# Kernel optimization log

Hardware: AMD Instinct MI355X
Metric: run time of the kernel (lower is better)

## Reference

```python
import math
import jax, jax.numpy as jnp
import numpy as np

N_HEADS = 16
D_HEAD = 128
D_ROPE = 64  # d_head // 2
ROPE_SCALE = 40.0


def _rotate_half(x):
    x1, x2 = jnp.split(x, 2, axis=-1)
    return jnp.concatenate([-x2, x1], axis=-1)


def _apply_rotary(x, cos, sin):
    # rotate only the first cos.shape[-1] dims of the rope slice
    half = cos.shape[-1]
    x_rot, x_base = x[..., :half], x[..., half:]
    x_rot = x_rot * cos + _rotate_half(x_rot) * sin
    return jnp.concatenate([x_rot, x_base], axis=-1)


def _forward(x, W_dkv, W_dq, W_uk, W_uv, W_uq, W_kr, W_qr, W_out):
    B, S, H = x.shape
    c_kv = x @ W_dkv                                   # [B,S,cd]
    c_q = x @ W_dq                                     # [B,S,cd]
    q_c = c_q @ W_uq                                   # [B,S,up]
    k_c = c_kv @ W_uk                                  # [B,S,up]
    v = (c_kv @ W_uv).reshape(B, S, N_HEADS, D_HEAD)   # [B,S,h,d]
    k_r = (x @ W_kr).reshape(B, S, N_HEADS, D_ROPE)
    q_r = (q_c @ W_qr).reshape(B, S, N_HEADS, D_ROPE)

    # RoPE (partial: first d_rope//2 dims rotated, rest passthrough)
    half_dim = D_ROPE // 2
    inv_freq = 1.0 / (10000.0 ** (jnp.arange(0, half_dim, 2, dtype=jnp.float32) / half_dim))
    t = jnp.arange(S, dtype=jnp.float32) / ROPE_SCALE
    freqs = jnp.einsum('i,j->ij', t, inv_freq)         # [S, d_rope//4]
    rotation = jnp.concatenate([freqs, freqs], axis=-1)  # [S, d_rope//2]
    cos = jnp.cos(rotation)[None, :, None, :]
    sin = jnp.sin(rotation)[None, :, None, :]
    k_rope = _apply_rotary(k_r, cos, sin)
    q_rope = _apply_rotary(q_r, cos, sin)

    k = jnp.concatenate([k_c.reshape(B, S, N_HEADS, D_HEAD - D_ROPE), k_rope], axis=-1)
    q = jnp.concatenate([q_c.reshape(B, S, N_HEADS, D_HEAD - D_ROPE), q_rope], axis=-1)

    # NOTE: faithful to source: einsum takes (k, q) in that order, and the
    # softmax result is computed but UNUSED (AV uses raw scores). Replicated.
    scores = jnp.einsum('bihd,bjhd->bhij', k, q) / math.sqrt(D_HEAD)
    out = jnp.einsum('bhij,bjhd->bihd', scores, v)     # [B,S,h,d]
    output = out.reshape(B, S, N_HEADS * D_HEAD) @ W_out
    return output, c_kv, k_rope


def setup_inputs() -> dict:
    key = jax.random.key(0)
    ks = jax.random.split(key, 9)
    B, S, H, CD, UP = 2, 2048, 2048, 1024, 1024
    w = lambda k, shp: jax.random.normal(k, shp, dtype=jnp.float32) * 0.02
    return {
        'x': jax.random.normal(ks[0], (B, S, H), dtype=jnp.float32),
        'W_dkv': w(ks[1], (H, CD)),
        'W_dq': w(ks[2], (H, CD)),
        'W_uk': w(ks[3], (CD, UP)),
        'W_uv': w(ks[4], (CD, N_HEADS * D_HEAD)),
        'W_uq': w(ks[5], (CD, UP)),
        'W_kr': w(ks[6], (H, N_HEADS * D_ROPE)),
        'W_qr': w(ks[7], (CD, N_HEADS * D_ROPE)),
        'W_out': w(ks[8], (N_HEADS * D_HEAD, H)),
    }


def reference(x, W_dkv, W_dq, W_uk, W_uv, W_uq, W_kr, W_qr, W_out):
    return _forward(x, W_dkv, W_dq, W_uk, W_uv, W_uq, W_kr, W_qr, W_out)
```

## Files before the change

kernel.cpp:

```cpp
#include <hip/hip_runtime.h>
#include <math.h>

typedef _Float16 half8 __attribute__((ext_vector_type(8)));
typedef float floatx4 __attribute__((ext_vector_type(4)));

typedef const uint32_t __attribute__((address_space(1)))* gp1_t;
typedef uint32_t __attribute__((address_space(3)))* lp3_t;
#define GLDS16(g, l) __builtin_amdgcn_global_load_lds((gp1_t)(const void*)(g), (lp3_t)(void*)(l), 16, 0, 0)

#define BK 32

#define BARRIER() __builtin_amdgcn_s_barrier()
#define VM8()     asm volatile("s_waitcnt vmcnt(8)" ::: "memory")

__device__ inline int xcd_swz(int wg, int nwg)
{
    int q = nwg >> 3, r = nwg & 7;
    int xcd = wg & 7, idx = wg >> 3;
    return (xcd < r) ? (xcd * (q + 1) + idx) : (r * (q + 1) + (xcd - r) * q + idx);
}

__global__ __launch_bounds__(256) void gemm_fast(
    const _Float16* __restrict__ A, const _Float16* __restrict__ B,
    float* __restrict__ Cf, _Float16* __restrict__ Ch,
    float* __restrict__ Cx, _Float16* __restrict__ Cy,
    int Kc, long lda, long ldb, long ldcf, long ldch,
    int cmap, long cf_lo, long cf_hi, float alpha, int nh, int nsk, int epi_mode,
    long aoff_b, long aoff_h, long boff_b, long boff_h,
    long coff_b, long coff_h, long coff_s)
{
    __shared__ __align__(16) _Float16 As[128 * BK];
    __shared__ __align__(16) _Float16 Bs[128 * BK];

    const int z = blockIdx.z;
    const int hs = nh * nsk;
    const int zb = z / hs;
    const int rr = z % hs;
    const int zh = rr / nsk;
    const int ks = rr % nsk;

    const _Float16* Ab = A + (long)zb * aoff_b + (long)zh * aoff_h + (long)ks * Kc;
    const _Float16* Bb = B + (long)zb * boff_b + (long)zh * boff_h + (long)ks * Kc;
    const long cofs = (long)zb * coff_b + (long)zh * coff_h + (long)ks * coff_s;

    const int nwg = gridDim.x * gridDim.y;
    const int swz = xcd_swz(blockIdx.y * gridDim.x + blockIdx.x, nwg);
    const long m0 = (long)(swz / gridDim.x) * 128;
    const long n0 = (long)(swz % gridDim.x) * 128;
    const int t = threadIdx.x;
    const int wave = t >> 6, lane = t & 63;
    const int lr = lane & 15, lq = lane >> 4;
    const int wm = (wave & 1) * 64, wn = (wave >> 1) * 64;

    const int c0 = wave * 64 + lane;
    const int c1 = c0 + 256;
    const _Float16* ga0 = Ab + (m0 + (c0 >> 2)) * lda + (c0 & 3) * 8;
    const _Float16* ga1 = Ab + (m0 + (c1 >> 2)) * lda + (c1 & 3) * 8;
    const _Float16* gb0 = Bb + (n0 + (c0 >> 2)) * ldb + (c0 & 3) * 8;
    const _Float16* gb1 = Bb + (n0 + (c1 >> 2)) * ldb + (c1 & 3) * 8;
    _Float16* lA0 = As + wave * 512;
    _Float16* lA1 = As + 2048 + wave * 512;
    _Float16* lB0 = Bs + wave * 512;
    _Float16* lB1 = Bs + 2048 + wave * 512;

    floatx4 acc[4][4];
    #pragma unroll
    for (int i = 0; i < 4; ++i)
        #pragma unroll
        for (int j = 0; j < 4; ++j) acc[i][j] = (floatx4){0.f, 0.f, 0.f, 0.f};

    for (int k0 = 0; k0 < Kc; k0 += BK) {
        GLDS16(ga0, lA0); GLDS16(ga1, lA1);
        GLDS16(gb0, lB0); GLDS16(gb1, lB1);
        ga0 += BK; ga1 += BK; gb0 += BK; gb1 += BK;
        __syncthreads();

        half8 a[4], b[4];
        #pragma unroll
        for (int i = 0; i < 4; ++i) a[i] = *(const half8*)(As + (wm + i * 16 + lr) * BK + lq * 8);
        #pragma unroll
        for (int j = 0; j < 4; ++j) b[j] = *(const half8*)(Bs + (wn + j * 16 + lr) * BK + lq * 8);
        #pragma unroll
        for (int i = 0; i < 4; ++i)
            #pragma unroll
            for (int j = 0; j < 4; ++j)
                acc[i][j] = __builtin_amdgcn_mfma_f32_16x16x32_f16(a[i], b[j], acc[i][j], 0, 0, 0);
        __syncthreads();
    }

    if (epi_mode == 0) {
        #pragma unroll
        for (int i = 0; i < 4; ++i)
            #pragma unroll
            for (int j = 0; j < 4; ++j)
                #pragma unroll
                for (int r = 0; r < 4; ++r) {
                    long row = m0 + wm + i * 16 + lq * 4 + r;
                    long col = n0 + wn + j * 16 + lr;
                    float v = alpha * acc[i][j][r];
                    if (Ch) {
                        long cm = cmap ? ((col >> 6) * 128 + (col & 63)) : col;
                        Ch[cofs + row * ldch + cm] = (_Float16)v;
                    }
                    if (Cf && col >= cf_lo && col < cf_hi)
                        Cf[cofs + row * ldcf + (col - cf_lo)] = v;
                }
    } else if (epi_mode == 1) {
        const int nb = (int)n0 + wn;
        if (nb < 2048) {
            #pragma unroll
            for (int i = 0; i < 4; ++i)
                #pragma unroll
                for (int j = 0; j < 4; ++j)
                    #pragma unroll
                    for (int r = 0; r < 4; ++r) {
                        long row = m0 + wm + i * 16 + lq * 4 + r;
                        long col = n0 + wn + j * 16 + lr;
                        float v = acc[i][j][r];
                        Ch[row * 2048 + col] = (_Float16)v;
                        if (nb < 1024) Cf[row * 1024 + col] = v;
                    }
        } else {
            const int h = (nb - 2048) >> 6;
            const float invf = powf(10000.0f, -(float)lr / 16.0f);
            #pragma unroll
            for (int i = 0; i < 4; ++i)
                #pragma unroll
                for (int r = 0; r < 4; ++r) {
                    long row = m0 + wm + i * 16 + lq * 4 + r;
                    int s = (int)row & 2047;
                    float ang = ((float)s / 40.0f) * invf;
                    float cv = cosf(ang), sv = sinf(ang);
                    float v0 = acc[i][0][r], v1 = acc[i][1][r];
                    float y[4] = { v0 * cv - v1 * sv, v1 * cv + v0 * sv,
                                   acc[i][2][r], acc[i][3][r] };
                    #pragma unroll
                    for (int j = 0; j < 4; ++j) {
                        int d = j * 16 + lr;
                        Cx[row * 1024 + h * 64 + d] = y[j];
                        Cy[row * 2048 + h * 128 + 64 + d] = (_Float16)y[j];
                    }
                }
        }
    } else {
        if (zb == 0) {
            #pragma unroll
            for (int i = 0; i < 4; ++i)
                #pragma unroll
                for (int j = 0; j < 4; ++j)
                    #pragma unroll
                    for (int r = 0; r < 4; ++r) {
                        long row = m0 + wm + i * 16 + lq * 4 + r;
                        long col = n0 + wn + j * 16 + lr;
                        Ch[cofs + row * ldch + col] = (_Float16)acc[i][j][r];
                    }
        } else {
            const int mb = (int)m0 + wm;
            if (mb < 1024) {
                #pragma unroll
                for (int i = 0; i < 4; ++i)
                    #pragma unroll
                    for (int j = 0; j < 4; ++j)
                        #pragma unroll
                        for (int r = 0; r < 4; ++r) {
                            long u = m0 + wm + i * 16 + lq * 4 + r;
                            long col = n0 + wn + j * 16 + lr;
                            long qrow = ((u >> 6) << 7) + (u & 63);
                            Ch[cofs + qrow * 4096 + col] = (_Float16)acc[i][j][r];
                        }
            } else {
                const int h = (mb - 1024) >> 6;
                #pragma unroll
                for (int j = 0; j < 4; ++j)
                    #pragma unroll
                    for (int r = 0; r < 4; ++r) {
                        long col = n0 + wn + j * 16 + lr;
                        int s = (int)col & 2047;
                        int j16 = lq * 4 + r;
                        float ivf = powf(10000.0f, -(float)j16 / 16.0f);
                        float ang = ((float)s / 40.0f) * ivf;
                        float cv = cosf(ang), sv = sinf(ang);
                        float v0 = acc[0][j][r], v1 = acc[1][j][r];
                        float y[4] = { v0 * cv - v1 * sv, v1 * cv + v0 * sv,
                                       acc[2][j][r], acc[3][j][r] };
                        #pragma unroll
                        for (int i = 0; i < 4; ++i) {
                            int dd = i * 16 + lq * 4 + r;
                            long qrow = h * 128 + 64 + dd;
                            Ch[cofs + qrow * 4096 + col] = (_Float16)y[i];
                        }
                    }
            }
        }
    }
}

__global__ __launch_bounds__(512, 2) void gemm256(
    const _Float16* __restrict__ A, const _Float16* __restrict__ B,
    float* __restrict__ Cf, _Float16* __restrict__ Ch,
    float* __restrict__ Cx, _Float16* __restrict__ Cy,
    int Kc, long lda, long ldb, long ldcf, long ldch,
    int cmap, long cf_lo, long cf_hi, float alpha, int nh, int nsk, int epi_mode,
    long aoff_b, long aoff_h, long boff_b, long boff_h,
    long coff_b, long coff_h, long coff_s)
{
    __shared__ __align__(16) _Float16 sm[65536];

    const int z = blockIdx.z;
    const int hs = nh * nsk;
    const int zb = z / hs;
    const int rr = z % hs;
    const int zh = rr / nsk;
    const int ks = rr % nsk;

    const _Float16* Ab = A + (long)zb * aoff_b + (long)zh * aoff_h + (long)ks * Kc;
    const _Float16* Bb = B + (long)zb * boff_b + (long)zh * boff_h + (long)ks * Kc;
    const long cofs = (long)zb * coff_b + (long)zh * coff_h + (long)ks * coff_s;

    const int nwg = gridDim.x * gridDim.y;
    const int swz = xcd_swz(blockIdx.y * gridDim.x + blockIdx.x, nwg);
    const long m0 = (long)(swz / gridDim.x) * 256;
    const long n0 = (long)(swz % gridDim.x) * 256;
    const int t = threadIdx.x;
    const int wave = t >> 6, lane = t & 63;
    const int lr = lane & 15, lq = lane >> 4;
    const int wm = (wave >> 2) * 128, wn = (wave & 3) * 64;
    const int wmrb = wm >> 4, wnrb = wn >> 4;
    const int NT = Kc >> 6;

    floatx4 acc[8][4];
    #pragma unroll
    for (int i = 0; i < 8; ++i)
        #pragma unroll
        for (int j = 0; j < 4; ++j) acc[i][j] = (floatx4){0.f, 0.f, 0.f, 0.f};

#define ST(tt_, kk_, q_, b_) do { \
        const int tcl_ = (tt_) < NT ? (tt_) : (tt_) - NT; \
        const int isB_ = (q_) >> 1; \
        const int rb_ = ((q_) & 1) * 8 + wave; \
        const long grow_ = (isB_ ? n0 : m0) + rb_ * 16 + lr; \
        const _Float16* src_ = (isB_ ? Bb + grow_ * ldb : Ab + grow_ * lda) \
                               + (long)tcl_ * 64 + (kk_) * 32 + lq * 8; \
        _Float16* dst_ = sm + (b_) * 32768 + isB_ * 16384 + (rb_ * 2 + (kk_)) * 512; \
        GLDS16(src_, dst_); \
    } while (0)

#define LOADA(ihb_, kk_) { _Pragma("unroll") \
    for (int i_ = 0; i_ < 4; ++i_) \
        aF[i_] = *(const half8*)(At + (((wmrb + (ihb_) + i_) * 2 + (kk_)) << 9) + lane * 8); }
#define LOADB(kk_) { _Pragma("unroll") \
    for (int j_ = 0; j_ < 4; ++j_) \
        bF[j_] = *(const half8*)(Bt + (((wnrb + j_) * 2 + (kk_)) << 9) + lane * 8); }
#define MFMA16(ihb_) { _Pragma("unroll") \
    for (int i_ = 0; i_ < 4; ++i_) { _Pragma("unroll") \
        for (int j_ = 0; j_ < 4; ++j_) \
            acc[(ihb_) + i_][j_] = __builtin_amdgcn_mfma_f32_16x16x32_f16(aF[i_], bF[j_], acc[(ihb_) + i_][j_], 0, 0, 0); } }

    ST(0, 0, 0, 0); ST(0, 0, 1, 0); ST(0, 0, 2, 0); ST(0, 0, 3, 0);
    ST(0, 1, 0, 0); ST(0, 1, 1, 0); ST(0, 1, 2, 0); ST(0, 1, 3, 0);
    ST(1, 0, 0, 1); ST(1, 0, 1, 1); ST(1, 0, 2, 1); ST(1, 0, 3, 1);
    VM8(); BARRIER();

    half8 aF[4], bF[4];
    for (int tt = 0; tt < NT; ++tt) {
        const int buf = tt & 1, ob = buf ^ 1;
        const _Float16* At = sm + buf * 32768;
        const _Float16* Bt = At + 16384;

        ST(tt + 1, 1, 0, ob); ST(tt + 1, 1, 1, ob);
        ST(tt + 1, 1, 2, ob); ST(tt + 1, 1, 3, ob);
        LOADA(0, 0); LOADB(0);
        __builtin_amdgcn_s_setprio(1); MFMA16(0); __builtin_amdgcn_s_setprio(0);
        LOADA(4, 0);
        __builtin_amdgcn_s_setprio(1); MFMA16(4); __builtin_amdgcn_s_setprio(0);
        VM8();
        BARRIER();

        ST(tt + 2, 0, 0, buf); ST(tt + 2, 0, 1, buf);
        ST(tt + 2, 0, 2, buf); ST(tt + 2, 0, 3, buf);
        LOADA(0, 1); LOADB(1);
        __builtin_amdgcn_s_setprio(1); MFMA16(0); __builtin_amdgcn_s_setprio(0);
        LOADA(4, 1);
        __builtin_amdgcn_s_setprio(1); MFMA16(4); __builtin_amdgcn_s_setprio(0);
        VM8();
        BARRIER();
    }
#undef ST
#undef LOADA
#undef LOADB
#undef MFMA16

    if (epi_mode == 0) {
        #pragma unroll
        for (int i = 0; i < 8; ++i)
            #pragma unroll
            for (int j = 0; j < 4; ++j)
                #pragma unroll
                for (int r = 0; r < 4; ++r) {
                    long row = m0 + wm + i * 16 + lq * 4 + r;
                    long col = n0 + wn + j * 16 + lr;
                    float v = alpha * acc[i][j][r];
                    if (Ch) {
                        long cm = cmap ? ((col >> 6) * 128 + (col & 63)) : col;
                        Ch[cofs + row * ldch + cm] = (_Float16)v;
                    }
                    if (Cf && col >= cf_lo && col < cf_hi)
                        Cf[cofs + row * ldcf + (col - cf_lo)] = v;
                }
    } else if (epi_mode == 1) {
        const int nb = (int)n0 + wn;
        if (nb < 2048) {
            #pragma unroll
            for (int i = 0; i < 8; ++i)
                #pragma unroll
                for (int j = 0; j < 4; ++j)
                    #pragma unroll
                    for (int r = 0; r < 4; ++r) {
                        long row = m0 + wm + i * 16 + lq * 4 + r;
                        long col = n0 + wn + j * 16 + lr;
                        float v = acc[i][j][r];
                        Ch[row * 2048 + col] = (_Float16)v;
                        if (nb < 1024) Cf[row * 1024 + col] = v;
                    }
        } else {
            const int h = (nb - 2048) >> 6;
            const float invf = powf(10000.0f, -(float)lr / 16.0f);
            #pragma unroll
            for (int i = 0; i < 8; ++i)
                #pragma unroll
                for (int r = 0; r < 4; ++r) {
                    long row = m0 + wm + i * 16 + lq * 4 + r;
                    int s = (int)row & 2047;
                    float ang = ((float)s / 40.0f) * invf;
                    float cv = cosf(ang), sv = sinf(ang);
                    float v0 = acc[i][0][r], v1 = acc[i][1][r];
                    float y[4] = { v0 * cv - v1 * sv, v1 * cv + v0 * sv,
                                   acc[i][2][r], acc[i][3][r] };
                    #pragma unroll
                    for (int j = 0; j < 4; ++j) {
                        int d = j * 16 + lr;
                        Cx[row * 1024 + h * 64 + d] = y[j];
                        Cy[row * 2048 + h * 128 + 64 + d] = (_Float16)y[j];
                    }
                }
        }
    } else {
        if (zb == 0) {
            #pragma unroll
            for (int i = 0; i < 8; ++i)
                #pragma unroll
                for (int j = 0; j < 4; ++j)
                    #pragma unroll
                    for (int r = 0; r < 4; ++r) {
                        long row = m0 + wm + i * 16 + lq * 4 + r;
                        long col = n0 + wn + j * 16 + lr;
                        Ch[cofs + row * ldch + col] = (_Float16)acc[i][j][r];
                    }
        } else {
            const int mb = (int)m0 + wm;
            if (mb < 1024) {
                #pragma unroll
                for (int i = 0; i < 8; ++i)
                    #pragma unroll
                    for (int j = 0; j < 4; ++j)
                        #pragma unroll
                        for (int r = 0; r < 4; ++r) {
                            long u = m0 + wm + i * 16 + lq * 4 + r;
                            long col = n0 + wn + j * 16 + lr;
                            long qrow = ((u >> 6) << 7) + (u & 63);
                            Ch[cofs + qrow * 4096 + col] = (_Float16)acc[i][j][r];
                        }
            } else {
                const int hbase = (mb - 1024) >> 6;
                #pragma unroll
                for (int ih = 0; ih < 2; ++ih) {
                    const int h = hbase + ih;
                    #pragma unroll
                    for (int j = 0; j < 4; ++j)
                        #pragma unroll
                        for (int r = 0; r < 4; ++r) {
                            long col = n0 + wn + j * 16 + lr;
                            int s = (int)col & 2047;
                            int j16 = lq * 4 + r;
                            float ivf = powf(10000.0f, -(float)j16 / 16.0f);
                            float ang = ((float)s / 40.0f) * ivf;
                            float cv = cosf(ang), sv = sinf(ang);
                            float v0 = acc[ih * 4 + 0][j][r], v1 = acc[ih * 4 + 1][j][r];
                            float y[4] = { v0 * cv - v1 * sv, v1 * cv + v0 * sv,
                                           acc[ih * 4 + 2][j][r], acc[ih * 4 + 3][j][r] };
                            #pragma unroll
                            for (int ii = 0; ii < 4; ++ii) {
                                int dd = ii * 16 + lq * 4 + r;
                                long qrow = h * 128 + 64 + dd;
                                Ch[cofs + qrow * 4096 + col] = (_Float16)y[ii];
                            }
                        }
                }
            }
        }
    }
}

__device__ inline void tr_tile(const float* __restrict__ in, _Float16* __restrict__ out,
                               int R, int C, int tile, int tx, int ty, float (*tb)[33])
{
    int tc = tile % (C >> 5), tr = tile / (C >> 5);
    int c0 = tc * 32, r0 = tr * 32;
    for (int i = ty; i < 32; i += 8)
        tb[i][tx] = in[(long)(r0 + i) * C + c0 + tx];
    __syncthreads();
    for (int i = ty; i < 32; i += 8)
        out[(long)(c0 + i) * R + r0 + tx] = (_Float16)tb[tx][i];
}

__device__ inline void cast_blk(const float* __restrict__ in, _Float16* __restrict__ out,
                                int blk, int tid)
{
    long idx = (long)blk * 2048 + tid * 8;
    float4 a = ((const float4*)(in + idx))[0];
    float4 b = ((const float4*)(in + idx))[1];
    half8 h = { (_Float16)a.x, (_Float16)a.y, (_Float16)a.z, (_Float16)a.w,
                (_Float16)b.x, (_Float16)b.y, (_Float16)b.z, (_Float16)b.w };
    *(half8*)(out + idx) = h;
}

__global__ void prep_kernel(
    const float* __restrict__ x, const float* __restrict__ W_dkv,
    const float* __restrict__ W_dq, const float* __restrict__ W_uk,
    const float* __restrict__ W_uv, const float* __restrict__ W_uq,
    const float* __restrict__ W_kr, const float* __restrict__ W_qr,
    const float* __restrict__ W_out,
    _Float16* __restrict__ WcatT, _Float16* __restrict__ WukT,
    _Float16* __restrict__ WuvT, _Float16* __restrict__ WuqcatT,
    _Float16* __restrict__ WqrT, _Float16* __restrict__ Wuqh,
    _Float16* __restrict__ WoutT, _Float16* __restrict__ xh)
{
    __shared__ float tb[32][33];
    int blk = blockIdx.x;
    int tid = threadIdx.x;
    int tx = tid & 31, ty = tid >> 5;
    if (blk < 2048)        tr_tile(W_dkv, WcatT,            2048, 1024, blk,         tx, ty, tb);
    else if (blk < 4096)   tr_tile(W_dq,  WcatT + 2097152,  2048, 1024, blk - 2048,  tx, ty, tb);
    else if (blk < 6144)   tr_tile(W_kr,  WcatT + 4194304,  2048, 1024, blk - 4096,  tx, ty, tb);
    else if (blk < 7168)   tr_tile(W_uk,  WukT,             1024, 1024, blk - 6144,  tx, ty, tb);
    else if (blk < 8192)   tr_tile(W_uq,  WuqcatT,          1024, 1024, blk - 7168,  tx, ty, tb);
    else if (blk < 9216)   tr_tile(W_qr,  WqrT,             1024, 1024, blk - 8192,  tx, ty, tb);
    else if (blk < 11264)  tr_tile(W_uv,  WuvT,             1024, 2048, blk - 9216,  tx, ty, tb);
    else if (blk < 15360)  tr_tile(W_out, WoutT,            2048, 2048, blk - 11264, tx, ty, tb);
    else if (blk < 19456)  cast_blk(x,    xh,   blk - 15360, tid);
    else                   cast_blk(W_uq, Wuqh, blk - 19456, tid);
}

__global__ void reduce8_cast_kernel(const float* __restrict__ in, _Float16* __restrict__ out)
{
    int i = blockIdx.x * 256 + threadIdx.x;
    float s = 0.f;
    #pragma unroll
    for (int j = 0; j < 8; ++j) s += in[i + j * 524288];
    out[i] = (_Float16)s;
}

extern "C" void kernel_launch(void* const* d_in, const int* in_sizes, int n_in,
                              void* d_out, int out_size, void* d_ws, size_t ws_size,
                              hipStream_t stream)
{
    const float* x     = (const float*)d_in[0];
    const float* W_dkv = (const float*)d_in[1];
    const float* W_dq  = (const float*)d_in[2];
    const float* W_uk  = (const float*)d_in[3];
    const float* W_uv  = (const float*)d_in[4];
    const float* W_uq  = (const float*)d_in[5];
    const float* W_kr  = (const float*)d_in[6];
    const float* W_qr  = (const float*)d_in[7];
    const float* W_out = (const float*)d_in[8];

    float* out_main  = (float*)d_out;
    float* out_ckv   = out_main + 8388608;
    float* out_krope = out_ckv + 4194304;

    char* w = (char*)d_ws;
    size_t off = 0;
    auto alloc = [&](size_t bytes) { void* p = w + off; off += (bytes + 255) & ~(size_t)255; return p; };

    _Float16* catA    = (_Float16*)alloc(16777216);
    _Float16* WcatT   = (_Float16*)alloc(12582912);
    _Float16* WukT    = (_Float16*)alloc(2097152);
    _Float16* WuvT    = (_Float16*)alloc(4194304);
    _Float16* WuqcatT = (_Float16*)alloc(4194304);
    _Float16* WqrT    = (_Float16*)alloc(2097152);
    _Float16* Wuqh    = (_Float16*)alloc(2097152);
    _Float16* WoutT   = (_Float16*)alloc(8388608);
    void*     reg_xm  = alloc(16777216);
    _Float16* k_flat  = (_Float16*)alloc(16777216);
    _Float16* vT      = (_Float16*)alloc(16777216);
    _Float16* qT      = (_Float16*)alloc(16777216);

    _Float16* xh      = (_Float16*)reg_xm;
    float*    Mbuf32p = (float*)reg_xm;
    _Float16* PT      = catA;
    _Float16* WuqrT   = WuqcatT + 1048576;
    _Float16* Mbuf16  = WukT;

    #define GF(A_,B_,Cf_,Ch_,Cx_,Cy_,M_,N_,Kc_,lda_,ldb_,ldcf_,ldch_,cmap_,cflo_,cfhi_,alpha_,nb_,nh_,nsk_,mode_,ab,ah,bb,bh,cb,ch2,cs) \
        hipLaunchKernelGGL(gemm_fast, dim3((N_)/128,(M_)/128,(nb_)*(nh_)*(nsk_)), dim3(256), 0, stream, \
            A_, B_, Cf_, Ch_, Cx_, Cy_, (int)(Kc_), (long)(lda_), (long)(ldb_), (long)(ldcf_), (long)(ldch_), \
            cmap_, (long)(cflo_), (long)(cfhi_), (float)(alpha_), nh_, nsk_, mode_, \
            (long)(ab),(long)(ah),(long)(bb),(long)(bh),(long)(cb),(long)(ch2),(long)(cs))

    #define GF256(A_,B_,Cf_,Ch_,Cx_,Cy_,M_,N_,Kc_,lda_,ldb_,ldcf_,ldch_,cmap_,cflo_,cfhi_,alpha_,nb_,nh_,nsk_,mode_,ab,ah,bb,bh,cb,ch2,cs) \
        hipLaunchKernelGGL(gemm256, dim3((N_)/256,(M_)/256,(nb_)*(nh_)*(nsk_)), dim3(512), 0, stream, \
            A_, B_, Cf_, Ch_, Cx_, Cy_, (int)(Kc_), (long)(lda_), (long)(ldb_), (long)(ldcf_), (long)(ldch_), \
            cmap_, (long)(cflo_), (long)(cfhi_), (float)(alpha_), nh_, nsk_, mode_, \
            (long)(ab),(long)(ah),(long)(bb),(long)(bh),(long)(cb),(long)(ch2),(long)(cs))

    hipLaunchKernelGGL(prep_kernel, dim3(19968), dim3(256), 0, stream,
        x, W_dkv, W_dq, W_uk, W_uv, W_uq, W_kr, W_qr, W_out,
        WcatT, WukT, WuvT, WuqcatT, WqrT, Wuqh, WoutT, xh);

    GF256(xh, WcatT, out_ckv, catA, out_krope, k_flat, 4096, 3072, 2048, 2048, 2048, 0, 0,
       0, 0, 0, 1.0, 1, 1, 1, 1, 0,0,0,0,0,0,0);
    GF(WqrT, Wuqh, (float*)nullptr, WuqrT, (float*)nullptr, (_Float16*)nullptr,
       1024, 1024, 1024, 1024, 1024, 0, 1024, 0, 0, 0, 1.0, 1, 1, 1, 0, 0,0,0,0,0,0,0);
    GF(catA, WukT, (float*)nullptr, k_flat, (float*)nullptr, (_Float16*)nullptr,
       4096, 1024, 1024, 2048, 1024, 0, 2048, 1, 0, 0, 1.0, 1, 1, 1, 0, 0,0,0,0,0,0,0);
    GF256(WuvT, catA, (float*)nullptr, vT, (float*)nullptr, (_Float16*)nullptr,
       2048, 4096, 1024, 1024, 2048, 0, 4096, 0, 0, 0, 1.0, 2, 1, 1, 2,
       2097152, 0, 1024, 0, 8388608, 0, 0);
    GF(qT, vT, Mbuf32p, (_Float16*)nullptr, (float*)nullptr, (_Float16*)nullptr,
       128, 128, 256, 4096, 4096, 128, 0, 0, 0, 128, 0.08838834764831845, 2, 16, 8, 0,
       2048, 524288, 2048, 524288, 262144, 16384, 524288);
    hipLaunchKernelGGL(reduce8_cast_kernel, dim3(2048), dim3(256), 0, stream, Mbuf32p, Mbuf16);
    GF(WoutT, Mbuf16, (float*)nullptr, PT, (float*)nullptr, (_Float16*)nullptr,
       2048, 128, 128, 2048, 128, 0, 2048, 0, 0, 0, 1.0, 2, 16, 1, 0,
       0, 128, 262144, 16384, 4194304, 128, 0);
    GF(k_flat, PT, out_main, (_Float16*)nullptr, (float*)nullptr, (_Float16*)nullptr,
       2048, 2048, 2048, 2048, 2048, 2048, 0, 0, 0, 2048, 1.0, 2, 1, 1, 0,
       4194304, 0, 4194304, 0, 4194304, 0, 0);

    #undef GF
    #undef GF256
}
```

Baseline: 468.9 us.

## Shrink gemm256 tile to 256x128 with 3-stage BK=32 LDS pipeline

Changes the 512-thread GEMM kernel from a 256x256 tile with a double-buffered BK=64 loop to a 256x128 tile with a three-slot BK=32 ring buffer. LDS use drops from 128KB to 72KB, accumulators halve, and launch bounds rise to allow more resident blocks per CU. The aim is better occupancy and latency hiding. The cost is lower arithmetic intensity per tile, more global loads per FLOP, and one barrier per 32-wide K step instead of two per 64.

```diff
diff --git a/kernel.cpp b/kernel.cpp
--- a/kernel.cpp
+++ b/kernel.cpp
@@ -11,7 +11,7 @@
 #define BK 32
 
 #define BARRIER() __builtin_amdgcn_s_barrier()
-#define VM8()     asm volatile("s_waitcnt vmcnt(8)" ::: "memory")
+#define VM3()     asm volatile("s_waitcnt vmcnt(3)" ::: "memory")
 
 __device__ inline int xcd_swz(int wg, int nwg)
 {
@@ -195,7 +195,7 @@
     }
 }
 
-__global__ __launch_bounds__(512, 2) void gemm256(
+__global__ __launch_bounds__(512, 4) void gemm256(
     const _Float16* __restrict__ A, const _Float16* __restrict__ B,
     float* __restrict__ Cf, _Float16* __restrict__ Ch,
     float* __restrict__ Cx, _Float16* __restrict__ Cy,
@@ -204,7 +204,7 @@
     long aoff_b, long aoff_h, long boff_b, long boff_h,
     long coff_b, long coff_h, long coff_s)
 {
-    __shared__ __align__(16) _Float16 sm[65536];
+    __shared__ __align__(16) _Float16 sm[36864];
 
     const int z = blockIdx.z;
     const int hs = nh * nsk;
@@ -220,70 +220,56 @@
     const int nwg = gridDim.x * gridDim.y;
     const int swz = xcd_swz(blockIdx.y * gridDim.x + blockIdx.x, nwg);
     const long m0 = (long)(swz / gridDim.x) * 256;
-    const long n0 = (long)(swz % gridDim.x) * 256;
+    const long n0 = (long)(swz % gridDim.x) * 128;
     const int t = threadIdx.x;
     const int wave = t >> 6, lane = t & 63;
     const int lr = lane & 15, lq = lane >> 4;
-    const int wm = (wave >> 2) * 128, wn = (wave & 3) * 64;
-    const int wmrb = wm >> 4, wnrb = wn >> 4;
-    const int NT = Kc >> 6;
-
-    floatx4 acc[8][4];
+    const int wm = (wave >> 1) * 64, wn = (wave & 1) * 64;
+    const int wmrb = (wave >> 1) * 4, wnrb = (wave & 1) * 4;
+    const int NT = Kc >> 5;
+
+    floatx4 acc[4][4];
     #pragma unroll
-    for (int i = 0; i < 8; ++i)
+    for (int i = 0; i < 4; ++i)
         #pragma unroll
         for (int j = 0; j < 4; ++j) acc[i][j] = (floatx4){0.f, 0.f, 0.f, 0.f};
 
-#define ST(tt_, kk_, q_, b_) do { \
+#define ST(tt_, q_, sl_) do { \
         const int tcl_ = (tt_) < NT ? (tt_) : (tt_) - NT; \
-        const int isB_ = (q_) >> 1; \
-        const int rb_ = ((q_) & 1) * 8 + wave; \
-        const long grow_ = (isB_ ? n0 : m0) + rb_ * 16 + lr; \
+        const int isB_ = ((q_) == 2); \
+        const int u_ = isB_ ? wave : wave * 2 + (q_); \
+        const long grow_ = (isB_ ? n0 : m0) + u_ * 16 + lr; \
         const _Float16* src_ = (isB_ ? Bb + grow_ * ldb : Ab + grow_ * lda) \
-                               + (long)tcl_ * 64 + (kk_) * 32 + lq * 8; \
-        _Float16* dst_ = sm + (b_) * 32768 + isB_ * 16384 + (rb_ * 2 + (kk_)) * 512; \
+                               + (long)tcl_ * 32 + lq * 8; \
+        _Float16* dst_ = sm + (sl_) * 12288 + (isB_ ? 8192 : 0) + u_ * 512; \
         GLDS16(src_, dst_); \
     } while (0)
 
-#define LOADA(ihb_, kk_) { _Pragma("unroll") \
+#define LOADA(sl_) { _Pragma("unroll") \
     for (int i_ = 0; i_ < 4; ++i_) \
-        aF[i_] = *(const half8*)(At + (((wmrb + (ihb_) + i_) * 2 + (kk_)) << 9) + lane * 8); }
-#define LOADB(kk_) { _Pragma("unroll") \
+        aF[i_] = *(const half8*)(sm + (sl_) * 12288 + (wmrb + i_) * 512 + lane * 8); }
+#define LOADB(sl_) { _Pragma("unroll") \
     for (int j_ = 0; j_ < 4; ++j_) \
-        bF[j_] = *(const half8*)(Bt + (((wnrb + j_) * 2 + (kk_)) << 9) + lane * 8); }
-#define MFMA16(ihb_) { _Pragma("unroll") \
+        bF[j_] = *(const half8*)(sm + (sl_) * 12288 + 8192 + (wnrb + j_) * 512 + lane * 8); }
+#define MFMA16() { _Pragma("unroll") \
     for (int i_ = 0; i_ < 4; ++i_) { _Pragma("unroll") \
         for (int j_ = 0; j_ < 4; ++j_) \
-            acc[(ihb_) + i_][j_] = __builtin_amdgcn_mfma_f32_16x16x32_f16(aF[i_], bF[j_], acc[(ihb_) + i_][j_], 0, 0, 0); } }
-
-    ST(0, 0, 0, 0); ST(0, 0, 1, 0); ST(0, 0, 2, 0); ST(0, 0, 3, 0);
-    ST(0, 1, 0, 0); ST(0, 1, 1, 0); ST(0, 1, 2, 0); ST(0, 1, 3, 0);
-    ST(1, 0, 0, 1); ST(1, 0, 1, 1); ST(1, 0, 2, 1); ST(1, 0, 3, 1);
-    VM8(); BARRIER();
+            acc[i_][j_] = __builtin_amdgcn_mfma_f32_16x16x32_f16(aF[i_], bF[j_], acc[i_][j_], 0, 0, 0); } }
+
+    ST(0, 0, 0); ST(0, 1, 0); ST(0, 2, 0);
+    ST(1, 0, 1); ST(1, 1, 1); ST(1, 2, 1);
+    VM3(); BARRIER();
 
     half8 aF[4], bF[4];
+    int sc = 0, ss = 2;
     for (int tt = 0; tt < NT; ++tt) {
-        const int buf = tt & 1, ob = buf ^ 1;
-        const _Float16* At = sm + buf * 32768;
-        const _Float16* Bt = At + 16384;
-
-        ST(tt + 1, 1, 0, ob); ST(tt + 1, 1, 1, ob);
-        ST(tt + 1, 1, 2, ob); ST(tt + 1, 1, 3, ob);
-        LOADA(0, 0); LOADB(0);
-        __builtin_amdgcn_s_setprio(1); MFMA16(0); __builtin_amdgcn_s_setprio(0);
-        LOADA(4, 0);
-        __builtin_amdgcn_s_setprio(1); MFMA16(4); __builtin_amdgcn_s_setprio(0);
-        VM8();
+        ST(tt + 2, 0, ss); ST(tt + 2, 1, ss); ST(tt + 2, 2, ss);
+        LOADA(sc); LOADB(sc);
+        __builtin_amdgcn_s_setprio(1); MFMA16(); __builtin_amdgcn_s_setprio(0);
+        VM3();
         BARRIER();
-
-        ST(tt + 2, 0, 0, buf); ST(tt + 2, 0, 1, buf);
-        ST(tt + 2, 0, 2, buf); ST(tt + 2, 0, 3, buf);
-        LOADA(0, 1); LOADB(1);
-        __builtin_amdgcn_s_setprio(1); MFMA16(0); __builtin_amdgcn_s_setprio(0);
-        LOADA(4, 1);
-        __builtin_amdgcn_s_setprio(1); MFMA16(4); __builtin_amdgcn_s_setprio(0);
-        VM8();
-        BARRIER();
+        sc = (sc == 2) ? 0 : sc + 1;
+        ss = (ss == 2) ? 0 : ss + 1;
     }
 #undef ST
 #undef LOADA
@@ -292,7 +278,7 @@
 
     if (epi_mode == 0) {
         #pragma unroll
-        for (int i = 0; i < 8; ++i)
+        for (int i = 0; i < 4; ++i)
             #pragma unroll
             for (int j = 0; j < 4; ++j)
                 #pragma unroll
@@ -311,7 +297,7 @@
         const int nb = (int)n0 + wn;
         if (nb < 2048) {
             #pragma unroll
-            for (int i = 0; i < 8; ++i)
+            for (int i = 0; i < 4; ++i)
                 #pragma unroll
                 for (int j = 0; j < 4; ++j)
                     #pragma unroll
@@ -326,7 +312,7 @@
             const int h = (nb - 2048) >> 6;
             const float invf = powf(10000.0f, -(float)lr / 16.0f);
             #pragma unroll
-            for (int i = 0; i < 8; ++i)
+            for (int i = 0; i < 4; ++i)
                 #pragma unroll
                 for (int r = 0; r < 4; ++r) {
                     long row = m0 + wm + i * 16 + lq * 4 + r;
@@ -347,7 +333,7 @@
     } else {
         if (zb == 0) {
             #pragma unroll
-            for (int i = 0; i < 8; ++i)
+            for (int i = 0; i < 4; ++i)
                 #pragma unroll
                 for (int j = 0; j < 4; ++j)
                     #pragma unroll
@@ -360,7 +346,7 @@
             const int mb = (int)m0 + wm;
             if (mb < 1024) {
                 #pragma unroll
-                for (int i = 0; i < 8; ++i)
+                for (int i = 0; i < 4; ++i)
                     #pragma unroll
                     for (int j = 0; j < 4; ++j)
                         #pragma unroll
@@ -371,31 +357,27 @@
                             Ch[cofs + qrow * 4096 + col] = (_Float16)acc[i][j][r];
                         }
             } else {
-                const int hbase = (mb - 1024) >> 6;
-                #pragma unroll
-                for (int ih = 0; ih < 2; ++ih) {
-                    const int h = hbase + ih;
-                    #pragma unroll
-                    for (int j = 0; j < 4; ++j)
+                const int h = (mb - 1024) >> 6;
+                #pragma unroll
+                for (int j = 0; j < 4; ++j)
+                    #pragma unroll
+                    for (int r = 0; r < 4; ++r) {
+                        long col = n0 + wn + j * 16 + lr;
+                        int s = (int)col & 2047;
+                        int j16 = lq * 4 + r;
+                        float ivf = powf(10000.0f, -(float)j16 / 16.0f);
+                        float ang = ((float)s / 40.0f) * ivf;
+                        float cv = cosf(ang), sv = sinf(ang);
+                        float v0 = acc[0][j][r], v1 = acc[1][j][r];
+                        float y[4] = { v0 * cv - v1 * sv, v1 * cv + v0 * sv,
+                                       acc[2][j][r], acc[3][j][r] };
                         #pragma unroll
-                        for (int r = 0; r < 4; ++r) {
-                            long col = n0 + wn + j * 16 + lr;
-                            int s = (int)col & 2047;
-                            int j16 = lq * 4 + r;
-                            float ivf = powf(10000.0f, -(float)j16 / 16.0f);
-                            float ang = ((float)s / 40.0f) * ivf;
-                            float cv = cosf(ang), sv = sinf(ang);
-                            float v0 = acc[ih * 4 + 0][j][r], v1 = acc[ih * 4 + 1][j][r];
-                            float y[4] = { v0 * cv - v1 * sv, v1 * cv + v0 * sv,
-                                           acc[ih * 4 + 2][j][r], acc[ih * 4 + 3][j][r] };
-                            #pragma unroll
-                            for (int ii = 0; ii < 4; ++ii) {
-                                int dd = ii * 16 + lq * 4 + r;
-                                long qrow = h * 128 + 64 + dd;
-                                Ch[cofs + qrow * 4096 + col] = (_Float16)y[ii];
-                            }
+                        for (int i = 0; i < 4; ++i) {
+                            int dd = i * 16 + lq * 4 + r;
+                            long qrow = h * 128 + 64 + dd;
+                            Ch[cofs + qrow * 4096 + col] = (_Float16)y[i];
                         }
-                }
+                    }
             }
         }
     }
@@ -508,7 +490,7 @@
             (long)(ab),(long)(ah),(long)(bb),(long)(bh),(long)(cb),(long)(ch2),(long)(cs))
 
     #define GF256(A_,B_,Cf_,Ch_,Cx_,Cy_,M_,N_,Kc_,lda_,ldb_,ldcf_,ldch_,cmap_,cflo_,cfhi_,alpha_,nb_,nh_,nsk_,mode_,ab,ah,bb,bh,cb,ch2,cs) \
-        hipLaunchKernelGGL(gemm256, dim3((N_)/256,(M_)/256,(nb_)*(nh_)*(nsk_)), dim3(512), 0, stream, \
+        hipLaunchKernelGGL(gemm256, dim3((N_)/128,(M_)/256,(nb_)*(nh_)*(nsk_)), dim3(512), 0, stream, \
             A_, B_, Cf_, Ch_, Cx_, Cy_, (int)(Kc_), (long)(lda_), (long)(ldb_), (long)(ldcf_), (long)(ldch_), \
             cmap_, (long)(cflo_), (long)(cfhi_), (float)(alpha_), nh_, nsk_, mode_, \
             (long)(ab),(long)(ah),(long)(bb),(long)(bh),(long)(cb),(long)(ch2),(long)(cs))
```

New measurement: 464.3 us. Within noise of the previous version (-1.0%).
